# Kernel optimization log

Measured on AMD Instinct MI355X. Metric: run time of the kernel, lower is better.

## Reference

```python
import jax, jax.numpy as jnp
import numpy as np

B, N, D = 2, 2048, 1024   # batch, seq, input_dim
H, DK, DV = 8, 128, 1024  # heads, qk_dim, v_dim (v_dim == input_dim for residual)


def setup_inputs() -> dict:
    key = jax.random.key(0)
    kx, kq, kk, kv = jax.random.split(key, 4)
    scale = 0.02
    x = jax.random.normal(kx, (B, N, D), dtype=jnp.float32)
    # torch nn.Linear weights are [out_features, in_features]; stacked over heads.
    Wq = jax.random.normal(kq, (H, DK, D), dtype=jnp.float32) * scale
    Wk = jax.random.normal(kk, (H, DK, D), dtype=jnp.float32) * scale
    Wv = jax.random.normal(kv, (H, DV, D), dtype=jnp.float32) * scale
    return {"x": x, "Wq": Wq, "Wk": Wk, "Wv": Wv}


def reference(x, Wq, Wk, Wv):
    # x: [B, N, D]; Wq/Wk: [H, DK, D]; Wv: [H, DV, D]
    n = x.shape[-2]
    Q = jnp.einsum('bnd,hed->bhne', x, Wq)  # [B,H,N,DK]
    K = jnp.einsum('bnd,hed->bhne', x, Wk)  # [B,H,N,DK]
    V = jnp.einsum('bnd,hvd->bhnv', x, Wv)  # [B,H,N,DV]
    scores = jnp.einsum('bhne,bhme->bhnm', Q, K)  # [B,H,N,N]
    # causal mask: masked entries set to mask_value=0.0, then relu, then /N
    causal = jnp.tril(jnp.ones((n, n), dtype=bool))
    sim = jnp.where(causal, jax.nn.relu(scores), jnp.float32(0.0)) / jnp.float32(n)
    # sum of per-head outputs added to residual
    head_out = jnp.einsum('bhnm,bhmv->bnv', sim, V)  # [B,N,DV]
    return x + head_out
```

## Files before the change

kernel.cpp:

```cpp
#include <hip/hip_runtime.h>

typedef __attribute__((ext_vector_type(8))) short bf16x8;
typedef __attribute__((ext_vector_type(4))) float floatx4;

__device__ __forceinline__ unsigned short f2bf(float f) {
  unsigned int u = __builtin_bit_cast(unsigned int, f);
  unsigned int r = (u + 0x7fffu + ((u >> 16) & 1u)) >> 16;
  return (unsigned short)r;
}

__device__ __forceinline__ unsigned int pack2(float a, float b) {
  return (unsigned int)f2bf(a) | ((unsigned int)f2bf(b) << 16);
}

__device__ __forceinline__ void gload16(const void* g, void* l) {
  __builtin_amdgcn_global_load_lds(
      (__attribute__((address_space(1))) void*)g,
      (__attribute__((address_space(3))) void*)l, 16, 0, 0);
}

__device__ __forceinline__ void barrier_lgkm() {
  asm volatile("s_waitcnt lgkmcnt(0)" ::: "memory");
  __builtin_amdgcn_s_barrier();
  __builtin_amdgcn_sched_barrier(0);
}

__global__ __launch_bounds__(256) void convert_all(
    const float4* __restrict__ x4,
    const float4* __restrict__ wq4, const float4* __restrict__ wk4,
    const float4* __restrict__ wv4,
    uint2* __restrict__ xb4, uint2* __restrict__ wqkb4, uint2* __restrict__ wvb4,
    float4* __restrict__ out4)
{
  const int NX = 2 * 2048 * 1024 / 4;
  const int NQK = 8 * 256 * 1024 / 4;
  const int NV = 8 * 1024 * 1024 / 4;
  const int total = NX + NQK + NV;
  const float inv_n = 1.0f / 2048.0f;
  for (int i = blockIdx.x * 256 + threadIdx.x; i < total; i += gridDim.x * 256) {
    float4 f; uint2* dst;
    if (i < NX) {
      f = x4[i]; dst = &xb4[i];
      out4[i] = f;
    } else if (i < NX + NQK) {
      int j = i - NX;
      int c = j & 255;
      int row = j >> 8;
      int h = row >> 8, r = row & 255;
      f = (r < 128) ? wq4[(h * 128 + r) * 256 + c] : wk4[(h * 128 + r - 128) * 256 + c];
      dst = &wqkb4[j];
    } else {
      int j = i - NX - NQK;
      f = wv4[j];
      f.x *= inv_n; f.y *= inv_n; f.z *= inv_n; f.w *= inv_n;
      dst = &wvb4[j];
    }
    uint2 p; p.x = pack2(f.x, f.y); p.y = pack2(f.z, f.w);
    *dst = p;
  }
}

__global__ __launch_bounds__(256) void init_out(const float4* __restrict__ x,
                                                float4* __restrict__ out, int n4) {
  for (int i = blockIdx.x * 256 + threadIdx.x; i < n4; i += gridDim.x * 256)
    out[i] = x[i];
}

__device__ __forceinline__ void gemm_body(
    const unsigned short* __restrict__ Ag,
    const unsigned short* __restrict__ Bg,
    unsigned short* __restrict__ C, long ld,
    unsigned short* LA, unsigned short* LB, int t)
{
  const int l = t & 63, w = t >> 6;
  const int wr = w >> 1, wc = w & 1;
  const int l16 = l & 15, lq = l >> 4;
  floatx4 acc[4][4] = {};
  for (int k0 = 0; k0 < 1024; k0 += 64) {
    __syncthreads();
    for (int i = 0; i < 4; i++) {
      int cbase = i * 256 + (t & 192);
      int chunk = cbase + (t & 63);
      int row = chunk >> 3, c8 = chunk & 7;
      gload16(Ag + (long)row * 1024 + k0 + c8 * 8, &LA[cbase * 8]);
      gload16(Bg + (long)row * 1024 + k0 + c8 * 8, &LB[cbase * 8]);
    }
    __syncthreads();
    for (int kk = 0; kk < 2; kk++) {
      bf16x8 af[4], bfr[4];
      for (int m = 0; m < 4; m++)
        af[m]  = *reinterpret_cast<const bf16x8*>(&LA[(wr * 64 + m * 16 + l16) * 64 + kk * 32 + lq * 8]);
      for (int n = 0; n < 4; n++)
        bfr[n] = *reinterpret_cast<const bf16x8*>(&LB[(wc * 64 + n * 16 + l16) * 64 + kk * 32 + lq * 8]);
      for (int m = 0; m < 4; m++)
        for (int n = 0; n < 4; n++)
          acc[m][n] = __builtin_amdgcn_mfma_f32_16x16x32_bf16(af[m], bfr[n], acc[m][n], 0, 0, 0);
    }
  }
  for (int m = 0; m < 4; m++)
    for (int n = 0; n < 4; n++)
      for (int j = 0; j < 4; j++) {
        int row = wr * 64 + m * 16 + lq * 4 + j;
        int col = wc * 64 + n * 16 + l16;
        C[(long)row * ld + col] = f2bf(acc[m][n][j]);
      }
}

__global__ __launch_bounds__(256) void gemm_all(
    const unsigned short* __restrict__ xb,
    const unsigned short* __restrict__ Wqkb,
    const unsigned short* __restrict__ Wvb,
    unsigned short* __restrict__ Qb, unsigned short* __restrict__ Kb,
    unsigned short* __restrict__ Vtb)
{
  __shared__ __align__(16) unsigned short LA[128 * 64];
  __shared__ __align__(16) unsigned short LB[128 * 64];
  const int bid = blockIdx.x;
  const int t = threadIdx.x;
  if (bid < 512) {
    int bx = bid & 15, qy = (bid >> 4) & 1, z = bid >> 5;
    int b = z >> 3, h = z & 7;
    const unsigned short* Ag = xb + (long)b * 2048 * 1024 + (long)bx * 128 * 1024;
    const unsigned short* Bg = Wqkb + (long)h * 256 * 1024 + (long)qy * 128 * 1024;
    unsigned short* C = (qy ? Kb : Qb) + (long)z * 2048 * 128 + (long)bx * 128 * 128;
    gemm_body(Ag, Bg, C, 128, LA, LB, t);
  } else {
    int v = bid - 512;
    int bx = v & 7, by = (v >> 3) & 15, z = v >> 7;
    int b = z >> 3, h = z & 7;
    const unsigned short* Ag = Wvb + (long)h * 1024 * 1024 + (long)bx * 128 * 1024;
    const unsigned short* Bg = xb + (long)b * 2048 * 1024 + (long)by * 128 * 1024;
    unsigned short* C = Vtb + (long)z * 1024 * 2048 + (long)bx * 128 * 2048 + by * 128;
    gemm_body(Ag, Bg, C, 2048, LA, LB, t);
  }
}

__global__ __launch_bounds__(256) void gemm_bt(
    const float* __restrict__ Abase, long sAb, long sAh,
    const float* __restrict__ Bbase, long sBb, long sBh,
    unsigned short* __restrict__ Cbase, long sC,
    int M, int Nc, int K, int H, float cscale)
{
  int z = blockIdx.z;
  int b = z / H, h = z % H;
  const float* A  = Abase + (long)b * sAb + (long)h * sAh;
  const float* Bm = Bbase + (long)b * sBb + (long)h * sBh;
  unsigned short* C = Cbase + (long)z * sC;
  int tRow = blockIdx.x * 128;
  int tCol = blockIdx.y * 128;
  __shared__ __align__(16) unsigned short LA[128 * 72];
  __shared__ __align__(16) unsigned short LB[128 * 72];
  int t = threadIdx.x;
  int l = t & 63, w = t >> 6;
  int wr = w >> 1, wc = w & 1;
  int l16 = l & 15, lq = l >> 4;
  floatx4 acc[4][4] = {};
  for (int k0 = 0; k0 < K; k0 += 64) {
    __syncthreads();
    for (int i = 0; i < 8; i++) {
      int lin = i * 256 + t;
      int row = lin >> 4;
      int c4  = lin & 15;
      float4 va = *reinterpret_cast<const float4*>(A + (long)(tRow + row) * K + k0 + c4 * 4);
      uint2 pa; pa.x = pack2(va.x, va.y); pa.y = pack2(va.z, va.w);
      *reinterpret_cast<uint2*>(&LA[row * 72 + c4 * 4]) = pa;
      float4 vb = *reinterpret_cast<const float4*>(Bm + (long)(tCol + row) * K + k0 + c4 * 4);
      uint2 pb; pb.x = pack2(vb.x, vb.y); pb.y = pack2(vb.z, vb.w);
      *reinterpret_cast<uint2*>(&LB[row * 72 + c4 * 4]) = pb;
    }
    __syncthreads();
    for (int kk = 0; kk < 2; kk++) {
      bf16x8 af[4], bfr[4];
      for (int m = 0; m < 4; m++)
        af[m]  = *reinterpret_cast<const bf16x8*>(&LA[(wr * 64 + m * 16 + l16) * 72 + kk * 32 + lq * 8]);
      for (int n = 0; n < 4; n++)
        bfr[n] = *reinterpret_cast<const bf16x8*>(&LB[(wc * 64 + n * 16 + l16) * 72 + kk * 32 + lq * 8]);
      for (int m = 0; m < 4; m++)
        for (int n = 0; n < 4; n++)
          acc[m][n] = __builtin_amdgcn_mfma_f32_16x16x32_bf16(af[m], bfr[n], acc[m][n], 0, 0, 0);
    }
  }
  for (int m = 0; m < 4; m++)
    for (int n = 0; n < 4; n++)
      for (int j = 0; j < 4; j++) {
        int row = tRow + wr * 64 + m * 16 + lq * 4 + j;
        int col = tCol + wc * 64 + n * 16 + l16;
        C[(long)row * Nc + col] = f2bf(acc[m][n][j] * cscale);
      }
}

__global__ __launch_bounds__(256) void gemm_qk(
    const float* __restrict__ x,
    const float* __restrict__ Wq, const float* __restrict__ Wk,
    unsigned short* __restrict__ Qb, unsigned short* __restrict__ Kb)
{
  int z = blockIdx.z;
  int b = z >> 3, h = z & 7;
  const float* A  = x + (long)b * 2048 * 1024;
  const float* Bm = (blockIdx.y ? Wk : Wq) + (long)h * 128 * 1024;
  unsigned short* C = (blockIdx.y ? Kb : Qb) + (long)z * 2048 * 128;
  int tRow = blockIdx.x * 128;
  __shared__ __align__(16) unsigned short LA[128 * 72];
  __shared__ __align__(16) unsigned short LB[128 * 72];
  int t = threadIdx.x;
  int l = t & 63, w = t >> 6;
  int wr = w >> 1, wc = w & 1;
  int l16 = l & 15, lq = l >> 4;
  floatx4 acc[4][4] = {};
  const int K = 1024;
  for (int k0 = 0; k0 < K; k0 += 64) {
    __syncthreads();
    for (int i = 0; i < 8; i++) {
      int lin = i * 256 + t;
      int row = lin >> 4;
      int c4  = lin & 15;
      float4 va = *reinterpret_cast<const float4*>(A + (long)(tRow + row) * K + k0 + c4 * 4);
      uint2 pa; pa.x = pack2(va.x, va.y); pa.y = pack2(va.z, va.w);
      *reinterpret_cast<uint2*>(&LA[row * 72 + c4 * 4]) = pa;
      float4 vb = *reinterpret_cast<const float4*>(Bm + (long)row * K + k0 + c4 * 4);
      uint2 pb; pb.x = pack2(vb.x, vb.y); pb.y = pack2(vb.z, vb.w);
      *reinterpret_cast<uint2*>(&LB[row * 72 + c4 * 4]) = pb;
    }
    __syncthreads();
    for (int kk = 0; kk < 2; kk++) {
      bf16x8 af[4], bfr[4];
      for (int m = 0; m < 4; m++)
        af[m]  = *reinterpret_cast<const bf16x8*>(&LA[(wr * 64 + m * 16 + l16) * 72 + kk * 32 + lq * 8]);
      for (int n = 0; n < 4; n++)
        bfr[n] = *reinterpret_cast<const bf16x8*>(&LB[(wc * 64 + n * 16 + l16) * 72 + kk * 32 + lq * 8]);
      for (int m = 0; m < 4; m++)
        for (int n = 0; n < 4; n++)
          acc[m][n] = __builtin_amdgcn_mfma_f32_16x16x32_bf16(af[m], bfr[n], acc[m][n], 0, 0, 0);
    }
  }
  for (int m = 0; m < 4; m++)
    for (int n = 0; n < 4; n++)
      for (int j = 0; j < 4; j++) {
        int row = tRow + wr * 64 + m * 16 + lq * 4 + j;
        int col = wc * 64 + n * 16 + l16;
        C[(long)row * 128 + col] = f2bf(acc[m][n][j]);
      }
}

__global__ __launch_bounds__(256) void attn_fused(
    const unsigned short* __restrict__ Qb,
    const unsigned short* __restrict__ Kb,
    const unsigned short* __restrict__ Vtb,
    float* __restrict__ out)
{
  const int bid = blockIdx.x;
  const int z = bid & 15;
  const int pair = (bid >> 4) & 15;
  const int vb = bid >> 8;
  const int b = z >> 3;
  const int t = threadIdx.x;
  const int l = t & 63, w = t >> 6;
  const int l16 = l & 15, lq = l >> 4;
  const int wm = w & 1, wn = w >> 1;
  const int swz = l16 & 7;

  __shared__ __align__(16) unsigned short LK[64 * 128];
  __shared__ __align__(16) unsigned short LV[256 * 64];
  __shared__ __align__(16) unsigned short LP[64 * 64];

  const unsigned short* Qz = Qb + (long)z * 2048 * 128;
  const unsigned short* Kh = Kb + (long)z * 2048 * 128;
  const unsigned short* Vh = Vtb + (long)z * 1024 * 2048 + (long)(vb * 256) * 2048;

  int ksrc[4], kdst[4];
#pragma unroll
  for (int i = 0; i < 4; i++) {
    int chunk = i * 256 + w * 64 + l;
    int r = chunk >> 4, c = chunk & 15;
    int cs = ((c & 7) ^ (r & 7)) | (c & 8);
    ksrc[i] = r * 128 + cs * 8;
    kdst[i] = (i * 256 + w * 64) * 8;
  }
  int vsrc[8], vdst[8];
#pragma unroll
  for (int i = 0; i < 8; i++) {
    int chunk = i * 256 + w * 64 + l;
    int r = chunk >> 3, c = chunk & 7;
    int cs = c ^ (r & 7);
    vsrc[i] = r * 2048 + cs * 8;
    vdst[i] = (i * 256 + w * 64) * 8;
  }

  for (int hf = 0; hf < 2; hf++) {
    const int T = hf ? (31 - pair) : pair;
    const unsigned short* Qh = Qz + (long)T * 64 * 128;
    bf16x8 aQ[2][4];
#pragma unroll
    for (int sn = 0; sn < 2; sn++)
#pragma unroll
      for (int ke = 0; ke < 4; ke++)
        aQ[sn][ke] = *reinterpret_cast<const bf16x8*>(
            Qh + (long)(wn * 32 + sn * 16 + l16) * 128 + ke * 32 + lq * 8);
    floatx4 acc[4][4] = {};
    for (int M = 0; M <= T; M++) {
      __syncthreads();
      const unsigned short* KhM = Kh + M * 8192;
      const unsigned short* VhM = Vh + M * 64;
#pragma unroll
      for (int i = 0; i < 4; i++)
        gload16(KhM + ksrc[i], &LK[kdst[i]]);
#pragma unroll
      for (int i = 0; i < 8; i++)
        gload16(VhM + vsrc[i], &LV[vdst[i]]);
      __syncthreads();
      floatx4 sacc[2][2] = {{{}, {}}, {{}, {}}};
      __builtin_amdgcn_s_setprio(1);
#pragma unroll
      for (int ke = 0; ke < 4; ke++) {
        bf16x8 kf[2];
#pragma unroll
        for (int sm = 0; sm < 2; sm++) {
          int chunk = 4 * ke + lq;
          kf[sm] = *reinterpret_cast<const bf16x8*>(
              &LK[(wm * 32 + sm * 16 + l16) * 128 +
                  ((((chunk & 7) ^ swz) | (chunk & 8)) * 8)]);
        }
#pragma unroll
        for (int sm = 0; sm < 2; sm++)
#pragma unroll
          for (int sn = 0; sn < 2; sn++)
            sacc[sm][sn] = __builtin_amdgcn_mfma_f32_16x16x32_bf16(
                kf[sm], aQ[sn][ke], sacc[sm][sn], 0, 0, 0);
      }
      __builtin_amdgcn_s_setprio(0);
      const bool diag = (M == T);
#pragma unroll
      for (int sm = 0; sm < 2; sm++)
#pragma unroll
        for (int sn = 0; sn < 2; sn++) {
          floatx4 v = sacc[sm][sn];
          float f0 = fmaxf(v[0], 0.0f), f1 = fmaxf(v[1], 0.0f);
          float f2 = fmaxf(v[2], 0.0f), f3 = fmaxf(v[3], 0.0f);
          if (diag) {
            int mm = wm * 32 + sm * 16 + lq * 4;
            int nn = wn * 32 + sn * 16 + l16;
            if (mm + 0 > nn) f0 = 0.0f;
            if (mm + 1 > nn) f1 = 0.0f;
            if (mm + 2 > nn) f2 = 0.0f;
            if (mm + 3 > nn) f3 = 0.0f;
          }
          unsigned int p0, p1;
          asm("v_cvt_pk_bf16_f32 %0, %1, %2" : "=v"(p0) : "v"(f0), "v"(f1));
          asm("v_cvt_pk_bf16_f32 %0, %1, %2" : "=v"(p1) : "v"(f2), "v"(f3));
          uint2 pk; pk.x = p0; pk.y = p1;
          int row = wn * 32 + sn * 16 + l16;
          int cs = wm * 32 + sm * 16 + lq * 4;
          *reinterpret_cast<uint2*>(
              &LP[row * 64 + (((cs >> 3) ^ (row & 7)) * 8) + (cs & 7)]) = pk;
        }
      barrier_lgkm();
      __builtin_amdgcn_s_setprio(1);
#pragma unroll
      for (int km = 0; km < 2; km++) {
        bf16x8 aP[4], bV[4];
#pragma unroll
        for (int nf = 0; nf < 4; nf++)
          aP[nf] = *reinterpret_cast<const bf16x8*>(
              &LP[(nf * 16 + l16) * 64 + (((4 * km + lq) ^ swz) * 8)]);
#pragma unroll
        for (int vf = 0; vf < 4; vf++)
          bV[vf] = *reinterpret_cast<const bf16x8*>(
              &LV[(w * 64 + vf * 16 + l16) * 64 + (((4 * km + lq) ^ swz) * 8)]);
#pragma unroll
        for (int nf = 0; nf < 4; nf++)
#pragma unroll
          for (int vf = 0; vf < 4; vf++)
            acc[nf][vf] = __builtin_amdgcn_mfma_f32_16x16x32_bf16(
                aP[nf], bV[vf], acc[nf][vf], 0, 0, 0);
      }
      __builtin_amdgcn_s_setprio(0);
    }
#pragma unroll
    for (int nf = 0; nf < 4; nf++)
#pragma unroll
      for (int vf = 0; vf < 4; vf++)
#pragma unroll
        for (int j = 0; j < 4; j++) {
          int n = T * 64 + nf * 16 + lq * 4 + j;
          int v = vb * 256 + w * 64 + vf * 16 + l16;
          long idx = ((long)b * 2048 + n) * 1024 + v;
          unsafeAtomicAdd(&out[idx], acc[nf][vf][j]);
        }
  }
}

extern "C" void kernel_launch(void* const* d_in, const int* in_sizes, int n_in,
                              void* d_out, int out_size, void* d_ws, size_t ws_size,
                              hipStream_t stream) {
  const float* x  = (const float*)d_in[0];
  const float* Wq = (const float*)d_in[1];
  const float* Wk = (const float*)d_in[2];
  const float* Wv = (const float*)d_in[3];
  float* out = (float*)d_out;
  const size_t MB = 1u << 20;
  dim3 blk(256);

  if (ws_size >= 104 * MB) {
    unsigned short* Vtb  = (unsigned short*)d_ws;
    unsigned short* Wqkb = (unsigned short*)d_ws;
    unsigned short* Qb   = (unsigned short*)((char*)d_ws + 64 * MB);
    unsigned short* Kb   = (unsigned short*)((char*)d_ws + 72 * MB);
    unsigned short* xb   = (unsigned short*)((char*)d_ws + 80 * MB);
    unsigned short* Wvb  = (unsigned short*)((char*)d_ws + 88 * MB);

    convert_all<<<dim3(2048), blk, 0, stream>>>(
        (const float4*)x, (const float4*)Wq, (const float4*)Wk, (const float4*)Wv,
        (uint2*)xb, (uint2*)Wqkb, (uint2*)Wvb, (float4*)out);
    gemm_all<<<dim3(2560), blk, 0, stream>>>(xb, Wqkb, Wvb, Qb, Kb, Vtb);
    attn_fused<<<dim3(1024), blk, 0, stream>>>(Qb, Kb, Vtb, out);
  } else {
    unsigned short* Qb  = (unsigned short*)d_ws;
    unsigned short* Kb  = Qb + (size_t)2 * 8 * 2048 * 128;
    unsigned short* Vtb = Kb + (size_t)2 * 8 * 2048 * 128;
    init_out<<<dim3(1024), blk, 0, stream>>>(
        (const float4*)x, (float4*)out, 2 * 2048 * 1024 / 4);
    gemm_qk<<<dim3(16, 2, 16), blk, 0, stream>>>(x, Wq, Wk, Qb, Kb);
    gemm_bt<<<dim3(8, 16, 16), blk, 0, stream>>>(
        Wv, 0, (long)1024 * 1024, x, (long)2048 * 1024, 0,
        Vtb, (long)1024 * 2048, 1024, 2048, 1024, 8, 1.0f / 2048.0f);
    attn_fused<<<dim3(1024), blk, 0, stream>>>(Qb, Kb, Vtb, out);
  }
}
```

Measured before the change: 299.7 us.

## Double-buffer K tiles in attention loop and reorder V-projection block mapping

The fused attention kernel now double-buffers the K tile in LDS. The next K tile is prefetched while the current one is consumed, and waits use vmcnt counters instead of full syncthreads pairs, so K load latency overlaps compute. A launch_bounds occupancy hint of 2 is added. The V-projection block index mapping is swapped so that consecutive blocks share the same Wv tile, which may improve cache reuse. The extra LDS for the second K buffer may limit occupancy, and the V tile is still loaded synchronously.

Result: no change. 298.7 us (-0.3%).

```diff
diff --git a/kernel.cpp b/kernel.cpp
--- a/kernel.cpp
+++ b/kernel.cpp
@@ -21,6 +21,12 @@
 
 __device__ __forceinline__ void barrier_lgkm() {
   asm volatile("s_waitcnt lgkmcnt(0)" ::: "memory");
+  __builtin_amdgcn_s_barrier();
+  __builtin_amdgcn_sched_barrier(0);
+}
+
+__device__ __forceinline__ void barrier_v0_lgkm() {
+  asm volatile("s_waitcnt vmcnt(0) lgkmcnt(0)" ::: "memory");
   __builtin_amdgcn_s_barrier();
   __builtin_amdgcn_sched_barrier(0);
 }
@@ -126,7 +132,7 @@
     gemm_body(Ag, Bg, C, 128, LA, LB, t);
   } else {
     int v = bid - 512;
-    int bx = v & 7, by = (v >> 3) & 15, z = v >> 7;
+    int by = v & 15, bx = (v >> 4) & 7, z = v >> 7;
     int b = z >> 3, h = z & 7;
     const unsigned short* Ag = Wvb + (long)h * 1024 * 1024 + (long)bx * 128 * 1024;
     const unsigned short* Bg = xb + (long)b * 2048 * 1024 + (long)by * 128 * 1024;
@@ -242,7 +248,7 @@
       }
 }
 
-__global__ __launch_bounds__(256) void attn_fused(
+__global__ __launch_bounds__(256, 2) void attn_fused(
     const unsigned short* __restrict__ Qb,
     const unsigned short* __restrict__ Kb,
     const unsigned short* __restrict__ Vtb,
@@ -259,7 +265,7 @@
   const int wm = w & 1, wn = w >> 1;
   const int swz = l16 & 7;
 
-  __shared__ __align__(16) unsigned short LK[64 * 128];
+  __shared__ __align__(16) unsigned short LK[2][64 * 128];
   __shared__ __align__(16) unsigned short LV[256 * 64];
   __shared__ __align__(16) unsigned short LP[64 * 64];
 
@@ -286,6 +292,7 @@
     vdst[i] = (i * 256 + w * 64) * 8;
   }
 
+  int cur = 0;
   for (int hf = 0; hf < 2; hf++) {
     const int T = hf ? (31 - pair) : pair;
     const unsigned short* Qh = Qz + (long)T * 64 * 128;
@@ -297,17 +304,25 @@
         aQ[sn][ke] = *reinterpret_cast<const bf16x8*>(
             Qh + (long)(wn * 32 + sn * 16 + l16) * 128 + ke * 32 + lq * 8);
     floatx4 acc[4][4] = {};
+#pragma unroll
+    for (int i = 0; i < 4; i++)
+      gload16(Kh + ksrc[i], &LK[cur][kdst[i]]);
     for (int M = 0; M <= T; M++) {
-      __syncthreads();
-      const unsigned short* KhM = Kh + M * 8192;
-      const unsigned short* VhM = Vh + M * 64;
-#pragma unroll
-      for (int i = 0; i < 4; i++)
-        gload16(KhM + ksrc[i], &LK[kdst[i]]);
+      barrier_v0_lgkm();
 #pragma unroll
       for (int i = 0; i < 8; i++)
-        gload16(VhM + vsrc[i], &LV[vdst[i]]);
-      __syncthreads();
+        gload16(Vh + M * 64 + vsrc[i], &LV[vdst[i]]);
+      if (M < T) {
+#pragma unroll
+        for (int i = 0; i < 4; i++)
+          gload16(Kh + (M + 1) * 8192 + ksrc[i], &LK[cur ^ 1][kdst[i]]);
+        asm volatile("s_waitcnt vmcnt(4)" ::: "memory");
+      } else {
+        asm volatile("s_waitcnt vmcnt(0)" ::: "memory");
+      }
+      __builtin_amdgcn_s_barrier();
+      __builtin_amdgcn_sched_barrier(0);
+      const unsigned short* LKc = LK[cur];
       floatx4 sacc[2][2] = {{{}, {}}, {{}, {}}};
       __builtin_amdgcn_s_setprio(1);
 #pragma unroll
@@ -317,8 +332,8 @@
         for (int sm = 0; sm < 2; sm++) {
           int chunk = 4 * ke + lq;
           kf[sm] = *reinterpret_cast<const bf16x8*>(
-              &LK[(wm * 32 + sm * 16 + l16) * 128 +
-                  ((((chunk & 7) ^ swz) | (chunk & 8)) * 8)]);
+              &LKc[(wm * 32 + sm * 16 + l16) * 128 +
+                   ((((chunk & 7) ^ swz) | (chunk & 8)) * 8)]);
         }
 #pragma unroll
         for (int sm = 0; sm < 2; sm++)
@@ -374,6 +389,7 @@
                 aP[nf], bV[vf], acc[nf][vf], 0, 0, 0);
       }
       __builtin_amdgcn_s_setprio(0);
+      cur ^= 1;
     }
 #pragma unroll
     for (int nf = 0; nf < 4; nf++)
```
